# Performance work log

Measured on AMD Instinct MI355X. Metric: run time of the kernel, lower is better.

## Reference

```python
import math
import jax, jax.numpy as jnp
import numpy as np

E = 8          # num_experts
H = 1024       # hidden_dim
F = 2048       # ffn_dim
TOP_K = 2
CAP_FACTOR = 1.25
B, S = 2, 2048


def setup_inputs() -> dict:
    key = jax.random.key(0)
    ks = jax.random.split(key, 7)
    xavier_gu = math.sqrt(2.0 / (H + F))
    return {
        "x": jax.random.normal(ks[0], (B, S, H), dtype=jnp.float32),
        "router_weight": 0.01 * jax.random.normal(ks[1], (H, E), dtype=jnp.float32),
        "w_gate": xavier_gu * jax.random.normal(ks[2], (E, H, F), dtype=jnp.float32),
        "w_up": xavier_gu * jax.random.normal(ks[3], (E, H, F), dtype=jnp.float32),
        "w_down": xavier_gu * jax.random.normal(ks[4], (E, F, H), dtype=jnp.float32),
        "ln_gamma": jnp.ones((H,), dtype=jnp.float32),
        "ln_beta": jnp.zeros((H,), dtype=jnp.float32),
    }


def _layernorm(x, g, b, eps=1e-5):
    mu = x.mean(-1, keepdims=True)
    var = ((x - mu) ** 2).mean(-1, keepdims=True)
    return (x - mu) / jnp.sqrt(var + eps) * g + b


def reference(x, router_weight, w_gate, w_up, w_down, ln_gamma, ln_beta):
    Bd, Sd, Hd = x.shape
    T = Bd * Sd
    cap = int(math.ceil(CAP_FACTOR * T / E))  # static capacity per expert

    residual = x
    tokens = _layernorm(x, ln_gamma, ln_beta).reshape(T, Hd)

    # ---- router: softmax + top-k + renormalize ----
    logits = tokens @ router_weight                      # (T, E) fp32
    probs = jax.nn.softmax(logits, axis=-1)
    wts, idx = jax.lax.top_k(probs, TOP_K)               # (T, K)
    wts = wts / wts.sum(-1, keepdims=True)

    # ---- dispatch: first-come-first-served up to capacity per expert ----
    mask_all = (idx[None, :, :] == jnp.arange(E)[:, None, None]).any(-1)  # (E, T)
    # stable argsort puts routed token indices (in order) first
    sel = jnp.argsort(jnp.where(mask_all, 0, 1), axis=1, stable=True)[:, :cap]  # (E, cap)
    valid = jnp.take_along_axis(mask_all, sel, axis=1)   # (E, cap)
    xin = tokens[sel] * valid[..., None]                 # (E, cap, H); zeros for empty slots

    # ---- grouped SwiGLU expert GEMMs ----
    gate = jax.nn.silu(jnp.einsum('ech,ehf->ecf', xin, w_gate))
    up = jnp.einsum('ech,ehf->ecf', xin, w_up)
    expert_outputs = jnp.einsum('ecf,efh->ech', gate * up, w_down)  # (E, cap, H)

    # ---- scatter-gather combine (slot = min(t, cap-1), per reference impl) ----
    slot = jnp.minimum(jnp.arange(T), cap - 1)           # (T,)
    gathered = expert_outputs[idx, slot[:, None]]        # (T, K, H)
    out = (wts[..., None] * gathered).sum(axis=1)        # (T, H)

    return out.reshape(Bd, Sd, Hd) + residual
```

## Files before the change

### kernel.cpp

```cpp
#include <hip/hip_runtime.h>
#include <hip/hip_bf16.h>

#define NE 8
#define NH 1024
#define NF 2048
#define NT 4096
#define CAP 640

typedef __bf16 bf16x8 __attribute__((ext_vector_type(8)));
typedef float f32x4 __attribute__((ext_vector_type(4)));

__device__ __forceinline__ ushort f2bf(float f) {
    union { float f; unsigned u; } v; v.f = f;
    unsigned r = (v.u + 0x7FFFu + ((v.u >> 16) & 1u)) >> 16;
    return (ushort)r;
}

__global__ __launch_bounds__(256) void k_ln_router(
    const float* __restrict__ x, const float* __restrict__ rw,
    const float* __restrict__ gamma, const float* __restrict__ beta,
    ushort* __restrict__ tok_bf, int* __restrict__ idx, float* __restrict__ wts)
{
    int t = blockIdx.x, tid = threadIdx.x;
    int lane = tid & 63, wid = tid >> 6;
    const float* xp = x + (size_t)t * NH;

    float4 v = *(const float4*)(xp + tid * 4);
    float xs[4] = {v.x, v.y, v.z, v.w};
    float s = xs[0] + xs[1] + xs[2] + xs[3];
    float q = xs[0]*xs[0] + xs[1]*xs[1] + xs[2]*xs[2] + xs[3]*xs[3];

    __shared__ float rs[4], rq[4], rl[4][8];
    #pragma unroll
    for (int o = 32; o; o >>= 1) { s += __shfl_xor(s, o); q += __shfl_xor(q, o); }
    if (lane == 0) { rs[wid] = s; rq[wid] = q; }
    __syncthreads();
    float S = rs[0] + rs[1] + rs[2] + rs[3];
    float Q = rq[0] + rq[1] + rq[2] + rq[3];
    float mean = S * (1.0f / NH);
    float var  = Q * (1.0f / NH) - mean * mean;
    float rstd = 1.0f / sqrtf(var + 1e-5f);

    float le[8] = {0,0,0,0,0,0,0,0};
    ushort tb[4];
    #pragma unroll
    for (int j = 0; j < 4; ++j) {
        int h = tid * 4 + j;
        float nh = (xs[j] - mean) * rstd * gamma[h] + beta[h];
        tb[j] = f2bf(nh);
        float4 r0 = *(const float4*)(rw + h * 8);
        float4 r1 = *(const float4*)(rw + h * 8 + 4);
        le[0] += nh * r0.x; le[1] += nh * r0.y; le[2] += nh * r0.z; le[3] += nh * r0.w;
        le[4] += nh * r1.x; le[5] += nh * r1.y; le[6] += nh * r1.z; le[7] += nh * r1.w;
    }
    union { ushort s2[4]; uint2 u2; } pk;
    pk.s2[0]=tb[0]; pk.s2[1]=tb[1]; pk.s2[2]=tb[2]; pk.s2[3]=tb[3];
    *(uint2*)(tok_bf + (size_t)t * NH + tid * 4) = pk.u2;

    #pragma unroll
    for (int o = 32; o; o >>= 1)
        #pragma unroll
        for (int e = 0; e < 8; ++e) le[e] += __shfl_xor(le[e], o);
    if (lane == 0)
        #pragma unroll
        for (int e = 0; e < 8; ++e) rl[wid][e] = le[e];
    __syncthreads();

    if (tid == 0) {
        float l[8];
        #pragma unroll
        for (int e = 0; e < 8; ++e) l[e] = rl[0][e] + rl[1][e] + rl[2][e] + rl[3][e];
        float mx = l[0];
        #pragma unroll
        for (int e = 1; e < 8; ++e) mx = fmaxf(mx, l[e]);
        float p[8], den = 0.f;
        #pragma unroll
        for (int e = 0; e < 8; ++e) { p[e] = expf(l[e] - mx); den += p[e]; }
        float rden = 1.0f / den;
        #pragma unroll
        for (int e = 0; e < 8; ++e) p[e] *= rden;
        int i0 = 0; float b0 = p[0];
        #pragma unroll
        for (int e = 1; e < 8; ++e) if (p[e] > b0) { b0 = p[e]; i0 = e; }
        int i1 = (i0 == 0) ? 1 : 0; float b1 = p[i1];
        #pragma unroll
        for (int e = 0; e < 8; ++e) if (e != i0 && p[e] > b1) { b1 = p[e]; i1 = e; }
        float sw = 1.0f / (b0 + b1);
        idx[2*t] = i0; idx[2*t+1] = i1;
        wts[2*t] = b0 * sw; wts[2*t+1] = b1 * sw;
    }
}

__global__ __launch_bounds__(1024) void k_build_sel(
    const int* __restrict__ idx, int* __restrict__ sel)
{
    int e = blockIdx.x, tid = threadIdx.x;
    int lane = tid & 63, wid = tid >> 6;
    __shared__ int wsum[16], wpre[16], sbase;
    if (tid < CAP) sel[e * CAP + tid] = -1;
    if (tid == 0) sbase = 0;
    __syncthreads();

    for (int ch = 0; ch < NT / 1024; ++ch) {
        int t = ch * 1024 + tid;
        int m = (idx[2*t] == e || idx[2*t+1] == e) ? 1 : 0;
        int v = m;
        #pragma unroll
        for (int d = 1; d < 64; d <<= 1) {
            int u = __shfl_up(v, d);
            if (lane >= d) v += u;
        }
        if (lane == 63) wsum[wid] = v;
        __syncthreads();
        if (tid < 16) {
            int ws = wsum[tid], wv = ws;
            #pragma unroll
            for (int d = 1; d < 16; d <<= 1) {
                int u = __shfl_up(wv, d);
                if (tid >= d) wv += u;
            }
            wpre[tid] = wv - ws;
        }
        __syncthreads();
        int base0 = sbase;
        int slot = base0 + wpre[wid] + v - m;
        if (m && slot < CAP) sel[e * CAP + slot] = t;
        __syncthreads();
        if (tid == 0) sbase = base0 + wpre[15] + wsum[15];
        __syncthreads();
    }
}

__global__ __launch_bounds__(256) void k_gather(
    const int* __restrict__ sel, const ushort* __restrict__ tok,
    ushort* __restrict__ xin)
{
    int sIdx = blockIdx.x;
    int tokid = sel[sIdx];
    uint2 v = make_uint2(0u, 0u);
    if (tokid >= 0)
        v = *(const uint2*)(tok + (size_t)tokid * NH + threadIdx.x * 4);
    *(uint2*)(xin + (size_t)sIdx * NH + threadIdx.x * 4) = v;
}

#define BPAD 40

__device__ __forceinline__ void stage_b_16(
    const float* __restrict__ Bp, ushort* __restrict__ Bl,
    int k0, int ldb, int bn, int bkh)
{
    union { ushort sh[8]; uint4 v; } p0, p1;
    #pragma unroll
    for (int j = 0; j < 8; ++j) p0.sh[j] = f2bf(Bp[(k0 + bkh + j) * ldb + bn]);
    #pragma unroll
    for (int j = 0; j < 8; ++j) p1.sh[j] = f2bf(Bp[(k0 + bkh + 8 + j) * ldb + bn]);
    *(uint4*)&Bl[bn * BPAD + bkh] = p0.v;
    *(uint4*)&Bl[bn * BPAD + bkh + 8] = p1.v;
}

__global__ __launch_bounds__(256) void k_gemm1(
    const ushort* __restrict__ xin, const float* __restrict__ wg,
    const float* __restrict__ wu, ushort* __restrict__ hb)
{
    int e = blockIdx.z, mb = blockIdx.y, nb = blockIdx.x;
    const ushort* A  = xin + (size_t)e * CAP * NH + (size_t)mb * 128 * NH;
    const float*  Bg = wg  + (size_t)e * NH * NF + nb * 128;
    const float*  Bu = wu  + (size_t)e * NH * NF + nb * 128;
    ushort* out = hb + (size_t)e * CAP * NF + (size_t)mb * 128 * NF + nb * 128;

    __shared__ __align__(16) ushort Al[128 * BPAD];
    __shared__ __align__(16) ushort Bgl[128 * BPAD];
    __shared__ __align__(16) ushort Bul[128 * BPAD];

    int tid = threadIdx.x, lane = tid & 63, wid = tid >> 6;
    int wm = wid >> 1, wn = wid & 1;
    int lr = lane & 15, lq = lane >> 4;
    int bn  = wid * 32 + (lane & 31);
    int bkh = (lane >> 5) * 16;

    f32x4 accg[4][4] = {}; f32x4 accu[4][4] = {};

    for (int k0 = 0; k0 < NH; k0 += 32) {
        #pragma unroll
        for (int i = 0; i < 2; ++i) {
            int L = tid + i * 256;
            int row = L >> 2, cg = (L & 3) * 8;
            uint4 av = *(const uint4*)(A + (size_t)row * NH + k0 + cg);
            *(uint4*)&Al[row * BPAD + cg] = av;
        }
        stage_b_16(Bg, Bgl, k0, NF, bn, bkh);
        stage_b_16(Bu, Bul, k0, NF, bn, bkh);
        __syncthreads();

        bf16x8 af[4], bgf[4], buf_[4];
        #pragma unroll
        for (int m = 0; m < 4; ++m)
            af[m] = *(const bf16x8*)&Al[(wm * 64 + m * 16 + lr) * BPAD + lq * 8];
        #pragma unroll
        for (int n = 0; n < 4; ++n) {
            bgf[n]  = *(const bf16x8*)&Bgl[(wn * 64 + n * 16 + lr) * BPAD + lq * 8];
            buf_[n] = *(const bf16x8*)&Bul[(wn * 64 + n * 16 + lr) * BPAD + lq * 8];
        }
        #pragma unroll
        for (int m = 0; m < 4; ++m)
            #pragma unroll
            for (int n = 0; n < 4; ++n) {
                accg[m][n] = __builtin_amdgcn_mfma_f32_16x16x32_bf16(af[m], bgf[n],  accg[m][n], 0, 0, 0);
                accu[m][n] = __builtin_amdgcn_mfma_f32_16x16x32_bf16(af[m], buf_[n], accu[m][n], 0, 0, 0);
            }
        __syncthreads();
    }

    #pragma unroll
    for (int m = 0; m < 4; ++m)
        #pragma unroll
        for (int n = 0; n < 4; ++n)
            #pragma unroll
            for (int r = 0; r < 4; ++r) {
                int row = wm * 64 + m * 16 + lq * 4 + r;
                int col = wn * 64 + n * 16 + lr;
                float g = accg[m][n][r], u = accu[m][n][r];
                float sg = g / (1.0f + expf(-g));
                out[(size_t)row * NF + col] = f2bf(sg * u);
            }
}

__global__ __launch_bounds__(256) void k_gemm2(
    const ushort* __restrict__ hb, const float* __restrict__ wd,
    float* __restrict__ eo)
{
    int e = blockIdx.z, mb = blockIdx.y, nb = blockIdx.x;
    const ushort* A = hb + (size_t)e * CAP * NF + (size_t)mb * 128 * NF;
    const float*  B = wd + (size_t)e * NF * NH + nb * 64;
    float* out = eo + (size_t)e * CAP * NH + (size_t)mb * 128 * NH + nb * 64;

    __shared__ __align__(16) ushort Al[128 * BPAD];
    __shared__ __align__(16) ushort Bl[64 * BPAD];

    int tid = threadIdx.x, lane = tid & 63, wid = tid >> 6;
    int wm = wid >> 1, wn = wid & 1;
    int lr = lane & 15, lq = lane >> 4;
    int bn = tid & 63;
    int bg = tid >> 6;

    f32x4 acc[4][2] = {};

    for (int k0 = 0; k0 < NF; k0 += 32) {
        #pragma unroll
        for (int i = 0; i < 2; ++i) {
            int L = tid + i * 256;
            int row = L >> 2, cg = (L & 3) * 8;
            uint4 av = *(const uint4*)(A + (size_t)row * NF + k0 + cg);
            *(uint4*)&Al[row * BPAD + cg] = av;
        }
        {
            union { ushort sh[8]; uint4 v; } p;
            #pragma unroll
            for (int j = 0; j < 8; ++j)
                p.sh[j] = f2bf(B[(k0 + bg * 8 + j) * NH + bn]);
            *(uint4*)&Bl[bn * BPAD + bg * 8] = p.v;
        }
        __syncthreads();

        bf16x8 af[4], bf_[2];
        #pragma unroll
        for (int m = 0; m < 4; ++m)
            af[m] = *(const bf16x8*)&Al[(wm * 64 + m * 16 + lr) * BPAD + lq * 8];
        #pragma unroll
        for (int n = 0; n < 2; ++n)
            bf_[n] = *(const bf16x8*)&Bl[(wn * 32 + n * 16 + lr) * BPAD + lq * 8];
        #pragma unroll
        for (int m = 0; m < 4; ++m)
            #pragma unroll
            for (int n = 0; n < 2; ++n)
                acc[m][n] = __builtin_amdgcn_mfma_f32_16x16x32_bf16(af[m], bf_[n], acc[m][n], 0, 0, 0);
        __syncthreads();
    }

    #pragma unroll
    for (int m = 0; m < 4; ++m)
        #pragma unroll
        for (int n = 0; n < 2; ++n)
            #pragma unroll
            for (int r = 0; r < 4; ++r) {
                int row = wm * 64 + m * 16 + lq * 4 + r;
                int col = wn * 32 + n * 16 + lr;
                out[(size_t)row * NH + col] = acc[m][n][r];
            }
}

__global__ __launch_bounds__(256) void k_final(
    const float* __restrict__ x, const float* __restrict__ eo,
    const int* __restrict__ idx, const float* __restrict__ wts,
    float* __restrict__ out)
{
    int t = blockIdx.x;
    int c = (t < CAP - 1) ? t : (CAP - 1);
    int e0 = idx[2*t], e1 = idx[2*t+1];
    float w0 = wts[2*t], w1 = wts[2*t+1];
    int h = threadIdx.x * 4;
    float4 xv = *(const float4*)(x + (size_t)t * NH + h);
    float4 a = *(const float4*)(eo + ((size_t)e0 * CAP + c) * NH + h);
    float4 b = *(const float4*)(eo + ((size_t)e1 * CAP + c) * NH + h);
    float4 o;
    o.x = xv.x + w0 * a.x + w1 * b.x;
    o.y = xv.y + w0 * a.y + w1 * b.y;
    o.z = xv.z + w0 * a.z + w1 * b.z;
    o.w = xv.w + w0 * a.w + w1 * b.w;
    *(float4*)(out + (size_t)t * NH + h) = o;
}

extern "C" void kernel_launch(void* const* d_in, const int* in_sizes, int n_in,
                              void* d_out, int out_size, void* d_ws, size_t ws_size,
                              hipStream_t stream)
{
    const float* x     = (const float*)d_in[0];
    const float* rw    = (const float*)d_in[1];
    const float* wg    = (const float*)d_in[2];
    const float* wu    = (const float*)d_in[3];
    const float* wd    = (const float*)d_in[4];
    const float* gamma = (const float*)d_in[5];
    const float* beta  = (const float*)d_in[6];
    float* out = (float*)d_out;

    char* ws = (char*)d_ws;
    ushort* tok_bf = (ushort*)(ws);
    ushort* xin    = (ushort*)(ws + 8388608);
    ushort* hb     = (ushort*)(ws + 18874368);
    float*  eo     = (float*) (ws + 39845888);
    int*    idx    = (int*)   (ws + 60817408);
    float*  wts    = (float*) (ws + 60850176);
    int*    sel    = (int*)   (ws + 60882944);

    k_ln_router<<<NT, 256, 0, stream>>>(x, rw, gamma, beta, tok_bf, idx, wts);
    k_build_sel<<<NE, 1024, 0, stream>>>(idx, sel);
    k_gather<<<NE * CAP, 256, 0, stream>>>(sel, tok_bf, xin);
    k_gemm1<<<dim3(NF / 128, CAP / 128, NE), 256, 0, stream>>>(xin, wg, wu, hb);
    k_gemm2<<<dim3(NH / 64, CAP / 128, NE), 256, 0, stream>>>(hb, wd, eo);
    k_final<<<NT, 256, 0, stream>>>(x, eo, idx, wts, out);
}
```

Before: 439.8 us.

## Pre-transpose weights to bf16 and stage GEMM tiles via global_load_lds

Adds a per-call transpose kernel that converts the fp32 gate, up and down weights into K-contiguous bf16 copies in workspace. Both expert GEMMs then load A and B tiles straight into LDS with 16-byte global_load_lds instead of strided scalar fp32 loads followed by in-register conversion. This removes the uncoalesced, column-strided weight reads and the conversion work from the GEMM inner loop. In exchange it adds a full extra read and write pass over all weights every call, and drops the LDS padding, which may cause bank conflicts on the fragment reads.

```diff
diff --git a/kernel.cpp b/kernel.cpp
--- a/kernel.cpp
+++ b/kernel.cpp
@@ -14,6 +14,43 @@
     union { float f; unsigned u; } v; v.f = f;
     unsigned r = (v.u + 0x7FFFu + ((v.u >> 16) & 1u)) >> 16;
     return (ushort)r;
+}
+
+__device__ __forceinline__ void glds16(const ushort* g, ushort* l) {
+    __builtin_amdgcn_global_load_lds((const __attribute__((address_space(1))) void*)g,
+                                     (__attribute__((address_space(3))) void*)l,
+                                     16, 0, 0);
+}
+
+__global__ __launch_bounds__(256) void k_transpose(
+    const float* __restrict__ in, ushort* __restrict__ out, int R, int C)
+{
+    int e = blockIdx.z;
+    int c0 = blockIdx.x * 64, r0 = blockIdx.y * 64;
+    in  += (size_t)e * R * C;
+    out += (size_t)e * R * C;
+
+    __shared__ __align__(16) ushort lds[64 * 72];
+    int t = threadIdx.x;
+    int rl = t >> 4;
+    int cl = (t & 15) * 4;
+
+    #pragma unroll
+    for (int i = 0; i < 4; ++i) {
+        int r = i * 16 + rl;
+        float4 v = *(const float4*)(in + (size_t)(r0 + r) * C + c0 + cl);
+        lds[(cl + 0) * 72 + r] = f2bf(v.x);
+        lds[(cl + 1) * 72 + r] = f2bf(v.y);
+        lds[(cl + 2) * 72 + r] = f2bf(v.z);
+        lds[(cl + 3) * 72 + r] = f2bf(v.w);
+    }
+    __syncthreads();
+
+    int c = t >> 2, rq = (t & 3) * 16;
+    uint4 a = *(const uint4*)&lds[c * 72 + rq];
+    uint4 b = *(const uint4*)&lds[c * 72 + rq + 8];
+    *(uint4*)(out + (size_t)(c0 + c) * R + r0 + rq)     = a;
+    *(uint4*)(out + (size_t)(c0 + c) * R + r0 + rq + 8) = b;
 }
 
 __global__ __launch_bounds__(256) void k_ln_router(
@@ -143,63 +180,47 @@
     *(uint2*)(xin + (size_t)sIdx * NH + threadIdx.x * 4) = v;
 }
 
-#define BPAD 40
-
-__device__ __forceinline__ void stage_b_16(
-    const float* __restrict__ Bp, ushort* __restrict__ Bl,
-    int k0, int ldb, int bn, int bkh)
-{
-    union { ushort sh[8]; uint4 v; } p0, p1;
-    #pragma unroll
-    for (int j = 0; j < 8; ++j) p0.sh[j] = f2bf(Bp[(k0 + bkh + j) * ldb + bn]);
-    #pragma unroll
-    for (int j = 0; j < 8; ++j) p1.sh[j] = f2bf(Bp[(k0 + bkh + 8 + j) * ldb + bn]);
-    *(uint4*)&Bl[bn * BPAD + bkh] = p0.v;
-    *(uint4*)&Bl[bn * BPAD + bkh + 8] = p1.v;
-}
-
 __global__ __launch_bounds__(256) void k_gemm1(
-    const ushort* __restrict__ xin, const float* __restrict__ wg,
-    const float* __restrict__ wu, ushort* __restrict__ hb)
+    const ushort* __restrict__ xin, const ushort* __restrict__ wgT,
+    const ushort* __restrict__ wuT, ushort* __restrict__ hb)
 {
     int e = blockIdx.z, mb = blockIdx.y, nb = blockIdx.x;
     const ushort* A  = xin + (size_t)e * CAP * NH + (size_t)mb * 128 * NH;
-    const float*  Bg = wg  + (size_t)e * NH * NF + nb * 128;
-    const float*  Bu = wu  + (size_t)e * NH * NF + nb * 128;
+    const ushort* Bg = wgT + (size_t)e * NF * NH + (size_t)nb * 128 * NH;
+    const ushort* Bu = wuT + (size_t)e * NF * NH + (size_t)nb * 128 * NH;
     ushort* out = hb + (size_t)e * CAP * NF + (size_t)mb * 128 * NF + nb * 128;
 
-    __shared__ __align__(16) ushort Al[128 * BPAD];
-    __shared__ __align__(16) ushort Bgl[128 * BPAD];
-    __shared__ __align__(16) ushort Bul[128 * BPAD];
+    __shared__ __align__(16) ushort Al[128 * 32];
+    __shared__ __align__(16) ushort Bgl[128 * 32];
+    __shared__ __align__(16) ushort Bul[128 * 32];
 
     int tid = threadIdx.x, lane = tid & 63, wid = tid >> 6;
     int wm = wid >> 1, wn = wid & 1;
     int lr = lane & 15, lq = lane >> 4;
-    int bn  = wid * 32 + (lane & 31);
-    int bkh = (lane >> 5) * 16;
+    int ldrow = lane >> 2;
+    int lcol  = (lane & 3) * 8;
 
     f32x4 accg[4][4] = {}; f32x4 accu[4][4] = {};
 
     for (int k0 = 0; k0 < NH; k0 += 32) {
         #pragma unroll
         for (int i = 0; i < 2; ++i) {
-            int L = tid + i * 256;
-            int row = L >> 2, cg = (L & 3) * 8;
-            uint4 av = *(const uint4*)(A + (size_t)row * NH + k0 + cg);
-            *(uint4*)&Al[row * BPAD + cg] = av;
-        }
-        stage_b_16(Bg, Bgl, k0, NF, bn, bkh);
-        stage_b_16(Bu, Bul, k0, NF, bn, bkh);
+            int row = i * 64 + wid * 16 + ldrow;
+            int lb  = i * 2048 + wid * 512;
+            glds16(A  + (size_t)row * NH + k0 + lcol, Al  + lb);
+            glds16(Bg + (size_t)row * NH + k0 + lcol, Bgl + lb);
+            glds16(Bu + (size_t)row * NH + k0 + lcol, Bul + lb);
+        }
         __syncthreads();
 
         bf16x8 af[4], bgf[4], buf_[4];
         #pragma unroll
         for (int m = 0; m < 4; ++m)
-            af[m] = *(const bf16x8*)&Al[(wm * 64 + m * 16 + lr) * BPAD + lq * 8];
+            af[m] = *(const bf16x8*)&Al[(wm * 64 + m * 16 + lr) * 32 + lq * 8];
         #pragma unroll
         for (int n = 0; n < 4; ++n) {
-            bgf[n]  = *(const bf16x8*)&Bgl[(wn * 64 + n * 16 + lr) * BPAD + lq * 8];
-            buf_[n] = *(const bf16x8*)&Bul[(wn * 64 + n * 16 + lr) * BPAD + lq * 8];
+            bgf[n]  = *(const bf16x8*)&Bgl[(wn * 64 + n * 16 + lr) * 32 + lq * 8];
+            buf_[n] = *(const bf16x8*)&Bul[(wn * 64 + n * 16 + lr) * 32 + lq * 8];
         }
         #pragma unroll
         for (int m = 0; m < 4; ++m)
@@ -226,49 +247,41 @@
 }
 
 __global__ __launch_bounds__(256) void k_gemm2(
-    const ushort* __restrict__ hb, const float* __restrict__ wd,
+    const ushort* __restrict__ hb, const ushort* __restrict__ wdT,
     float* __restrict__ eo)
 {
     int e = blockIdx.z, mb = blockIdx.y, nb = blockIdx.x;
-    const ushort* A = hb + (size_t)e * CAP * NF + (size_t)mb * 128 * NF;
-    const float*  B = wd + (size_t)e * NF * NH + nb * 64;
+    const ushort* A = hb  + (size_t)e * CAP * NF + (size_t)mb * 128 * NF;
+    const ushort* B = wdT + (size_t)e * NH * NF + (size_t)nb * 64 * NF;
     float* out = eo + (size_t)e * CAP * NH + (size_t)mb * 128 * NH + nb * 64;
 
-    __shared__ __align__(16) ushort Al[128 * BPAD];
-    __shared__ __align__(16) ushort Bl[64 * BPAD];
+    __shared__ __align__(16) ushort Al[128 * 32];
+    __shared__ __align__(16) ushort Bl[64 * 32];
 
     int tid = threadIdx.x, lane = tid & 63, wid = tid >> 6;
     int wm = wid >> 1, wn = wid & 1;
     int lr = lane & 15, lq = lane >> 4;
-    int bn = tid & 63;
-    int bg = tid >> 6;
+    int ldrow = lane >> 2;
+    int lcol  = (lane & 3) * 8;
 
     f32x4 acc[4][2] = {};
 
     for (int k0 = 0; k0 < NF; k0 += 32) {
         #pragma unroll
         for (int i = 0; i < 2; ++i) {
-            int L = tid + i * 256;
-            int row = L >> 2, cg = (L & 3) * 8;
-            uint4 av = *(const uint4*)(A + (size_t)row * NF + k0 + cg);
-            *(uint4*)&Al[row * BPAD + cg] = av;
-        }
-        {
-            union { ushort sh[8]; uint4 v; } p;
-            #pragma unroll
-            for (int j = 0; j < 8; ++j)
-                p.sh[j] = f2bf(B[(k0 + bg * 8 + j) * NH + bn]);
-            *(uint4*)&Bl[bn * BPAD + bg * 8] = p.v;
-        }
+            int row = i * 64 + wid * 16 + ldrow;
+            glds16(A + (size_t)row * NF + k0 + lcol, Al + i * 2048 + wid * 512);
+        }
+        glds16(B + (size_t)(wid * 16 + ldrow) * NF + k0 + lcol, Bl + wid * 512);
         __syncthreads();
 
         bf16x8 af[4], bf_[2];
         #pragma unroll
         for (int m = 0; m < 4; ++m)
-            af[m] = *(const bf16x8*)&Al[(wm * 64 + m * 16 + lr) * BPAD + lq * 8];
+            af[m] = *(const bf16x8*)&Al[(wm * 64 + m * 16 + lr) * 32 + lq * 8];
         #pragma unroll
         for (int n = 0; n < 2; ++n)
-            bf_[n] = *(const bf16x8*)&Bl[(wn * 32 + n * 16 + lr) * BPAD + lq * 8];
+            bf_[n] = *(const bf16x8*)&Bl[(wn * 32 + n * 16 + lr) * 32 + lq * 8];
         #pragma unroll
         for (int m = 0; m < 4; ++m)
             #pragma unroll
@@ -325,17 +338,24 @@
 
     char* ws = (char*)d_ws;
     ushort* tok_bf = (ushort*)(ws);
-    ushort* xin    = (ushort*)(ws + 8388608);
-    ushort* hb     = (ushort*)(ws + 18874368);
-    float*  eo     = (float*) (ws + 39845888);
-    int*    idx    = (int*)   (ws + 60817408);
-    float*  wts    = (float*) (ws + 60850176);
-    int*    sel    = (int*)   (ws + 60882944);
+    ushort* xin    = (ushort*)(ws +   8388608);
+    ushort* hb     = (ushort*)(ws +  18874368);
+    float*  eo     = (float*) (ws +  39845888);
+    ushort* wgT    = (ushort*)(ws +  60817408);
+    ushort* wuT    = (ushort*)(ws +  94371840);
+    ushort* wdT    = (ushort*)(ws + 127926272);
+    int*    idx    = (int*)   (ws + 161480704);
+    float*  wts    = (float*) (ws + 161513472);
+    int*    sel    = (int*)   (ws + 161546240);
+
+    k_transpose<<<dim3(NF / 64, NH / 64, NE), 256, 0, stream>>>(wg, wgT, NH, NF);
+    k_transpose<<<dim3(NF / 64, NH / 64, NE), 256, 0, stream>>>(wu, wuT, NH, NF);
+    k_transpose<<<dim3(NH / 64, NF / 64, NE), 256, 0, stream>>>(wd, wdT, NF, NH);
 
     k_ln_router<<<NT, 256, 0, stream>>>(x, rw, gamma, beta, tok_bf, idx, wts);
     k_build_sel<<<NE, 1024, 0, stream>>>(idx, sel);
     k_gather<<<NE * CAP, 256, 0, stream>>>(sel, tok_bf, xin);
-    k_gemm1<<<dim3(NF / 128, CAP / 128, NE), 256, 0, stream>>>(xin, wg, wu, hb);
-    k_gemm2<<<dim3(NH / 64, CAP / 128, NE), 256, 0, stream>>>(hb, wd, eo);
+    k_gemm1<<<dim3(NF / 128, CAP / 128, NE), 256, 0, stream>>>(xin, wgT, wuT, hb);
+    k_gemm2<<<dim3(NH / 64, CAP / 128, NE), 256, 0, stream>>>(hb, wdT, eo);
     k_final<<<NT, 256, 0, stream>>>(x, eo, idx, wts, out);
 }
```

Result: faster. 421.3 us (-4.2%).
